# Kernel tuning notes

Hardware: AMD Instinct MI355X
Metric: run time of the kernel (lower is better)

The kernel has to match this reference:

```python
import jax, jax.numpy as jnp
import numpy as np

N_NODES = 50000
N_EDGES = 1600000
CHANNELS = 128
EXPANSION = 50
CUTOFF = 5.0
LOG2 = 0.6931471805599453


def shifted_softplus(x):
    return jax.nn.softplus(x) - LOG2


def gaussian_smearing(r, cutoff=CUTOFF, n=EXPANSION):
    # centers evenly spaced in [0, cutoff]; width set by spacing
    centers = jnp.linspace(0.0, cutoff, n, dtype=r.dtype)
    delta = centers[1] - centers[0]
    coef = 1.0 / (2.0 * delta * delta)
    d = r[:, None] - centers[None, :]          # [E, n]
    return jnp.exp(-coef * d * d)


def setup_inputs() -> dict:
    key = jax.random.key(0)
    ks = jax.random.split(key, 12)
    C, F = CHANNELS, EXPANSION

    def lin(k, fan_in, shape):
        bound = 1.0 / np.sqrt(fan_in)
        return jax.random.uniform(k, shape, jnp.float32, -bound, bound)

    return {
        "features": jax.random.normal(ks[0], (N_NODES, C), jnp.float32),
        "edge_distances": jax.random.uniform(ks[1], (N_EDGES,), jnp.float32) * CUTOFF,
        "W_lin": lin(ks[2], C, (C, C)),
        "Wf1": lin(ks[3], F, (F, C)), "bf1": lin(ks[4], F, (C,)),
        "Wf2": lin(ks[5], C, (C, C)), "bf2": lin(ks[6], C, (C,)),
        "Wm1": lin(ks[7], C, (C, C)), "bm1": lin(ks[8], C, (C,)),
        "Wm2": lin(ks[9], C, (C, C)), "bm2": lin(ks[10], C, (C,)),
        "senders": jax.random.randint(ks[11], (N_EDGES,), 0, N_NODES, jnp.int32),
        "receivers": jax.random.randint(jax.random.fold_in(key, 99), (N_EDGES,), 0, N_NODES, jnp.int32),
    }


def reference(features, edge_distances, W_lin, Wf1, bf1, Wf2, bf2,
              Wm1, bm1, Wm2, bm2, senders, receivers):
    # 1. linear transform of node features (no bias)
    h = features @ W_lin.T                                   # [N, C]
    # 2. learnable radial filter F(r_ij): Gaussian basis -> MLP
    basis = gaussian_smearing(edge_distances)                # [E, F]
    ef = shifted_softplus(basis @ Wf1 + bf1) @ Wf2 + bf2     # [E, C]
    # 3. gather neighbour features, elementwise multiply, scatter-sum
    messages = h[senders] * ef                               # [E, C]
    agg = jax.ops.segment_sum(messages, receivers, num_segments=N_NODES)  # [N, C]
    # 4. output MLP
    return shifted_softplus(agg @ Wm1 + bm1) @ Wm2 + bm2
```

## Files before the change

### kernel.cpp

```cpp
#include <hip/hip_runtime.h>
#include <hip/hip_bf16.h>
#include <math.h>

#define N_NODES 50000
#define N_EDGES 1600000
#define CH 128
#define NF 50
#define NR 4096
#define NODES_PER_BLK 8
#define CHUNK 1024
#define NB 512
#define BUCKET_NODES 98
#define PASSA_CHUNK 4096
#define PASSB_CAP 4608

constexpr float DELTA  = 5.0f / 49.0f;
constexpr float COEF   = 1.0f / (2.0f * DELTA * DELTA);
constexpr float LOG2_  = 0.6931471805599453f;
constexpr float RSCALE = (float)(NR - 1) / 5.0f;

typedef short  bf16x8 __attribute__((ext_vector_type(8)));
typedef float  f32x4  __attribute__((ext_vector_type(4)));
typedef unsigned short ushort_t;
typedef unsigned long long u64;

__device__ __forceinline__ float ssp(float x) {
    return fmaxf(x, 0.0f) + __logf(1.0f + __expf(-fabsf(x))) - LOG2_;
}
__device__ __forceinline__ ushort_t f2bf(float x) {
    __hip_bfloat16 b = __float2bfloat16(x);
    return *reinterpret_cast<ushort_t*>(&b);
}
__device__ __forceinline__ float bf2f(ushort_t u) {
    return __uint_as_float(((unsigned)u) << 16);
}
__device__ __forceinline__ float4 f4zero() { return make_float4(0.f, 0.f, 0.f, 0.f); }

__global__ __launch_bounds__(256) void prep_weights(const float* __restrict__ Wlin,
                                                    const float* __restrict__ Wm1,
                                                    const float* __restrict__ Wm2,
                                                    ushort_t* __restrict__ wlhi,
                                                    ushort_t* __restrict__ wllo,
                                                    ushort_t* __restrict__ wm1hi,
                                                    ushort_t* __restrict__ wm1lo,
                                                    ushort_t* __restrict__ wm2hi,
                                                    ushort_t* __restrict__ wm2lo) {
    int idx = blockIdx.x * 256 + threadIdx.x;
    int n = idx >> 7, k = idx & 127;
    {   float w = Wlin[(size_t)n * CH + k];
        ushort_t hi = f2bf(w); wlhi[n * CH + k] = hi; wllo[n * CH + k] = f2bf(w - bf2f(hi)); }
    {   float w = Wm1[(size_t)k * CH + n];
        ushort_t hi = f2bf(w); wm1hi[n * CH + k] = hi; wm1lo[n * CH + k] = f2bf(w - bf2f(hi)); }
    {   float w = Wm2[(size_t)k * CH + n];
        ushort_t hi = f2bf(w); wm2hi[n * CH + k] = hi; wm2lo[n * CH + k] = f2bf(w - bf2f(hi)); }
}

__global__ __launch_bounds__(128) void table_build(const float* __restrict__ Wf1,
                                                   const float* __restrict__ bf1,
                                                   const float* __restrict__ Wf2,
                                                   const float* __restrict__ bf2,
                                                   float* __restrict__ tab) {
    __shared__ float bas[64];
    __shared__ float t1[128];
    const int g = blockIdx.x, tid = threadIdx.x;
    const float r = (float)g * (5.0f / (float)(NR - 1));
    if (tid < 64) {
        float v = 0.f;
        if (tid < NF) { float d = r - (float)tid * DELTA; v = __expf(-COEF * d * d); }
        bas[tid] = v;
    }
    __syncthreads();
    float acc = bf1[tid];
    for (int k = 0; k < NF; k++) acc = fmaf(bas[k], Wf1[k * CH + tid], acc);
    t1[tid] = ssp(acc);
    __syncthreads();
    float acc2 = bf2[tid];
    for (int k = 0; k < CH; k++) acc2 = fmaf(t1[k], Wf2[k * CH + tid], acc2);
    tab[(size_t)g * CH + tid] = acc2;
}

__global__ __launch_bounds__(256) void table_pack(const float* __restrict__ tab,
                                                  unsigned* __restrict__ tabi) {
    int idx = blockIdx.x * 256 + threadIdx.x;
    int g = idx >> 7, c = idx & 127;
    float a = tab[(size_t)g * CH + c];
    float b = tab[(size_t)min(g + 1, NR - 1) * CH + c];
    tabi[(size_t)g * CH + c] = (unsigned)f2bf(a) | ((unsigned)f2bf(b) << 16);
}

__global__ __launch_bounds__(256) void bucket_hist(const int* __restrict__ recv,
                                                   int* __restrict__ bcnt) {
    __shared__ int bh[NB];
    const int tid = threadIdx.x;
    for (int i = tid; i < NB; i += 256) bh[i] = 0;
    __syncthreads();
    const int e0 = blockIdx.x * PASSA_CHUNK;
#pragma unroll
    for (int i = 0; i < 16; i++) {
        int e = e0 + tid + i * 256;
        if (e < N_EDGES) atomicAdd(&bh[recv[e] / BUCKET_NODES], 1);
    }
    __syncthreads();
    for (int i = tid; i < NB; i += 256)
        if (bh[i]) atomicAdd(&bcnt[i], bh[i]);
}

__global__ __launch_bounds__(256) void bucket_scan(const int* __restrict__ bcnt,
                                                   int* __restrict__ bbase,
                                                   int* __restrict__ bcursor) {
    __shared__ int s[NB];
    const int tid = threadIdx.x;
    s[tid] = bcnt[tid];
    s[tid + 256] = bcnt[tid + 256];
    __syncthreads();
    if (tid == 0) {
        int acc = 0;
        for (int i = 0; i < NB; i++) { int c = s[i]; s[i] = acc; acc += c; }
    }
    __syncthreads();
    bbase[tid] = s[tid];           bbase[tid + 256] = s[tid + 256];
    bcursor[tid] = s[tid];         bcursor[tid + 256] = s[tid + 256];
    if (tid == 0) bbase[NB] = N_EDGES;
}

__global__ __launch_bounds__(256) void bucket_scatter(const int* __restrict__ recv,
                                                      const int* __restrict__ send,
                                                      const float* __restrict__ dist,
                                                      int* __restrict__ bcursor,
                                                      u64* __restrict__ brec) {
    __shared__ int bbaseL[NB];
    __shared__ int bcur[NB];
    const int tid = threadIdx.x;
    for (int i = tid; i < NB; i += 256) bcur[i] = 0;
    __syncthreads();
    const int e0 = blockIdx.x * PASSA_CHUNK;
#pragma unroll
    for (int i = 0; i < 16; i++) {
        int e = e0 + tid + i * 256;
        if (e < N_EDGES) atomicAdd(&bcur[recv[e] / BUCKET_NODES], 1);
    }
    __syncthreads();
    for (int i = tid; i < NB; i += 256) {
        int c = bcur[i];
        if (c) bbaseL[i] = atomicAdd(&bcursor[i], c);
        bcur[i] = 0;
    }
    __syncthreads();
#pragma unroll
    for (int i = 0; i < 16; i++) {
        int e = e0 + tid + i * 256;
        if (e < N_EDGES) {
            int r = recv[e];
            int b = r / BUCKET_NODES;
            int rank = atomicAdd(&bcur[b], 1);
            float x = fminf(dist[e] * RSCALE, (float)(NR - 1));
            u64 rec = (u64)(unsigned)(send[e] | (r << 16)) |
                      ((u64)__float_as_uint(x) << 32);
            brec[bbaseL[b] + rank] = rec;
        }
    }
}

__global__ __launch_bounds__(256) void bucket_sort(const int* __restrict__ bbase,
                                                   const u64* __restrict__ brec,
                                                   u64* __restrict__ meta,
                                                   int* __restrict__ cursor) {
    __shared__ int shist[BUCKET_NODES];
    __shared__ int sexc[BUCKET_NODES];
    __shared__ u64 sout[PASSB_CAP];
    const int b = blockIdx.x, tid = threadIdx.x;
    const int nbase = b * BUCKET_NODES;
    const int nn = min(BUCKET_NODES, N_NODES - nbase);
    if (nn <= 0) return;
    const int ebase = bbase[b], m = bbase[b + 1] - ebase;

    for (int i = tid; i < nn; i += 256) shist[i] = 0;
    __syncthreads();
    for (int i = tid; i < m; i += 256) {
        int l = (int)((brec[ebase + i] >> 16) & 0xFFFF) - nbase;
        atomicAdd(&shist[l], 1);
    }
    __syncthreads();
    if (tid == 0) {
        int acc = 0;
        for (int l = 0; l < nn; l++) { sexc[l] = acc; acc += shist[l]; }
    }
    __syncthreads();
    for (int l = tid; l < nn; l += 256)
        cursor[nbase + l] = ebase + sexc[l] + shist[l];
    __syncthreads();
    for (int i = tid; i < m; i += 256) {
        u64 rec = brec[ebase + i];
        int l = (int)((rec >> 16) & 0xFFFF) - nbase;
        int rank = atomicAdd(&sexc[l], 1);
        if (rank < PASSB_CAP) sout[rank] = rec;
    }
    __syncthreads();
    for (int i = tid; i < m; i += 256) meta[ebase + i] = sout[i];
}

__global__ __launch_bounds__(256) void dense_h(const float* __restrict__ X,
                                               const ushort_t* __restrict__ Bhi,
                                               const ushort_t* __restrict__ Blo,
                                               ushort_t* __restrict__ Y, int M) {
    __shared__ ushort_t xs[64][136];
    const int tid  = threadIdx.x;
    const int row0 = blockIdx.x * 64;

#pragma unroll
    for (int i = 0; i < 8; i++) {
        int idx = tid + i * 256;
        int r   = idx >> 5;
        int c4  = (idx & 31) * 4;
        float4 v = (row0 + r < M) ? *(const float4*)&X[(size_t)(row0 + r) * CH + c4]
                                  : f4zero();
        ushort4 s;
        s.x = f2bf(v.x); s.y = f2bf(v.y); s.z = f2bf(v.z); s.w = f2bf(v.w);
        *(ushort4*)&xs[r][c4] = s;
    }
    __syncthreads();

    const int lane = tid & 63;
    const int wv   = tid >> 6;
    const int row  = lane & 15;
    const int quad = lane >> 4;
    const int c0   = (2 * wv) * 16 + row;
    const int c1   = c0 + 16;

    f32x4 acc[2][4];
#pragma unroll
    for (int j = 0; j < 2; j++)
#pragma unroll
        for (int rt = 0; rt < 4; rt++) acc[j][rt] = (f32x4){0.f, 0.f, 0.f, 0.f};

#pragma unroll
    for (int kb = 0; kb < 128; kb += 32) {
        bf16x8 B0h = *(const bf16x8*)&Bhi[(size_t)c0 * CH + kb + quad * 8];
        bf16x8 B0l = *(const bf16x8*)&Blo[(size_t)c0 * CH + kb + quad * 8];
        bf16x8 B1h = *(const bf16x8*)&Bhi[(size_t)c1 * CH + kb + quad * 8];
        bf16x8 B1l = *(const bf16x8*)&Blo[(size_t)c1 * CH + kb + quad * 8];
#pragma unroll
        for (int rt = 0; rt < 4; rt++) {
            bf16x8 A = *(const bf16x8*)&xs[rt * 16 + row][kb + quad * 8];
            acc[0][rt] = __builtin_amdgcn_mfma_f32_16x16x32_bf16(A, B0l, acc[0][rt], 0, 0, 0);
            acc[0][rt] = __builtin_amdgcn_mfma_f32_16x16x32_bf16(A, B0h, acc[0][rt], 0, 0, 0);
            acc[1][rt] = __builtin_amdgcn_mfma_f32_16x16x32_bf16(A, B1l, acc[1][rt], 0, 0, 0);
            acc[1][rt] = __builtin_amdgcn_mfma_f32_16x16x32_bf16(A, B1h, acc[1][rt], 0, 0, 0);
        }
    }

#pragma unroll
    for (int j = 0; j < 2; j++) {
        int c = j ? c1 : c0;
#pragma unroll
        for (int rt = 0; rt < 4; rt++)
#pragma unroll
            for (int rg = 0; rg < 4; rg++) {
                int r = row0 + rt * 16 + quad * 4 + rg;
                if (r < M) Y[(size_t)r * CH + c] = f2bf(acc[j][rt][rg]);
            }
    }
}

__global__ __launch_bounds__(256) void out_mlp(const ushort_t* __restrict__ AGG,
                                               const ushort_t* __restrict__ B1hi,
                                               const ushort_t* __restrict__ B1lo,
                                               const float* __restrict__ bm1,
                                               const ushort_t* __restrict__ B2hi,
                                               const ushort_t* __restrict__ B2lo,
                                               const float* __restrict__ bm2,
                                               float* __restrict__ OUT, int M) {
    __shared__ ushort_t xs[64][136];
    __shared__ ushort_t ts[64][136];
    const int tid  = threadIdx.x;
    const int row0 = blockIdx.x * 64;

#pragma unroll
    for (int i = 0; i < 4; i++) {
        int idx = tid + i * 256;
        int r   = idx >> 4;
        int c8  = (idx & 15) * 8;
        uint4 v = (row0 + r < M) ? *(const uint4*)&AGG[(size_t)(row0 + r) * CH + c8]
                                 : make_uint4(0, 0, 0, 0);
        *(uint4*)&xs[r][c8] = v;
    }
    __syncthreads();

    const int lane = tid & 63;
    const int wv   = tid >> 6;
    const int row  = lane & 15;
    const int quad = lane >> 4;
    const int c0   = (2 * wv) * 16 + row;
    const int c1   = c0 + 16;

    f32x4 acc[2][4];
#pragma unroll
    for (int j = 0; j < 2; j++)
#pragma unroll
        for (int rt = 0; rt < 4; rt++) acc[j][rt] = (f32x4){0.f, 0.f, 0.f, 0.f};

#pragma unroll
    for (int kb = 0; kb < 128; kb += 32) {
        bf16x8 B0h = *(const bf16x8*)&B1hi[(size_t)c0 * CH + kb + quad * 8];
        bf16x8 B0l = *(const bf16x8*)&B1lo[(size_t)c0 * CH + kb + quad * 8];
        bf16x8 B1h_ = *(const bf16x8*)&B1hi[(size_t)c1 * CH + kb + quad * 8];
        bf16x8 B1l_ = *(const bf16x8*)&B1lo[(size_t)c1 * CH + kb + quad * 8];
#pragma unroll
        for (int rt = 0; rt < 4; rt++) {
            bf16x8 A = *(const bf16x8*)&xs[rt * 16 + row][kb + quad * 8];
            acc[0][rt] = __builtin_amdgcn_mfma_f32_16x16x32_bf16(A, B0l, acc[0][rt], 0, 0, 0);
            acc[0][rt] = __builtin_amdgcn_mfma_f32_16x16x32_bf16(A, B0h, acc[0][rt], 0, 0, 0);
            acc[1][rt] = __builtin_amdgcn_mfma_f32_16x16x32_bf16(A, B1l_, acc[1][rt], 0, 0, 0);
            acc[1][rt] = __builtin_amdgcn_mfma_f32_16x16x32_bf16(A, B1h_, acc[1][rt], 0, 0, 0);
        }
    }
    {
        float bv[2] = { bm1[c0], bm1[c1] };
#pragma unroll
        for (int j = 0; j < 2; j++) {
            int c = j ? c1 : c0;
#pragma unroll
            for (int rt = 0; rt < 4; rt++)
#pragma unroll
                for (int rg = 0; rg < 4; rg++)
                    ts[rt * 16 + quad * 4 + rg][c] = f2bf(ssp(acc[j][rt][rg] + bv[j]));
        }
    }
    __syncthreads();

#pragma unroll
    for (int j = 0; j < 2; j++)
#pragma unroll
        for (int rt = 0; rt < 4; rt++) acc[j][rt] = (f32x4){0.f, 0.f, 0.f, 0.f};

#pragma unroll
    for (int kb = 0; kb < 128; kb += 32) {
        bf16x8 B0h = *(const bf16x8*)&B2hi[(size_t)c0 * CH + kb + quad * 8];
        bf16x8 B0l = *(const bf16x8*)&B2lo[(size_t)c0 * CH + kb + quad * 8];
        bf16x8 B1h_ = *(const bf16x8*)&B2hi[(size_t)c1 * CH + kb + quad * 8];
        bf16x8 B1l_ = *(const bf16x8*)&B2lo[(size_t)c1 * CH + kb + quad * 8];
#pragma unroll
        for (int rt = 0; rt < 4; rt++) {
            bf16x8 A = *(const bf16x8*)&ts[rt * 16 + row][kb + quad * 8];
            acc[0][rt] = __builtin_amdgcn_mfma_f32_16x16x32_bf16(A, B0l, acc[0][rt], 0, 0, 0);
            acc[0][rt] = __builtin_amdgcn_mfma_f32_16x16x32_bf16(A, B0h, acc[0][rt], 0, 0, 0);
            acc[1][rt] = __builtin_amdgcn_mfma_f32_16x16x32_bf16(A, B1l_, acc[1][rt], 0, 0, 0);
            acc[1][rt] = __builtin_amdgcn_mfma_f32_16x16x32_bf16(A, B1h_, acc[1][rt], 0, 0, 0);
        }
    }
    {
        float bv[2] = { bm2[c0], bm2[c1] };
#pragma unroll
        for (int j = 0; j < 2; j++) {
            int c = j ? c1 : c0;
#pragma unroll
            for (int rt = 0; rt < 4; rt++)
#pragma unroll
                for (int rg = 0; rg < 4; rg++) {
                    int r = row0 + rt * 16 + quad * 4 + rg;
                    if (r < M) OUT[(size_t)r * CH + c] = acc[j][rt][rg] + bv[j];
                }
        }
    }
}

__global__ __launch_bounds__(256) void edge_gather(const int* __restrict__ cursor,
                                                   const u64* __restrict__ meta,
                                                   const ushort_t* __restrict__ h,
                                                   const unsigned* __restrict__ tabi,
                                                   ushort_t* __restrict__ aggb) {
    __shared__ u64 smeta[CHUNK];

    const int tid = threadIdx.x;
    const int n0  = blockIdx.x * NODES_PER_BLK;
    const int g   = tid >> 5;
    const int c4  = (tid & 31) * 4;
    const int n   = n0 + g;

    const int myend  = cursor[n];
    const int mybeg  = (n == 0) ? 0 : cursor[n - 1];
    const int blkbeg = (n0 == 0) ? 0 : cursor[n0 - 1];
    const int blkend = cursor[n0 + NODES_PER_BLK - 1];

    float4 macc = f4zero();

    for (int cs = blkbeg; cs < blkend; cs += CHUNK) {
        const int ce = min(cs + CHUNK, blkend);
        __syncthreads();
        for (int i = tid; i < ce - cs; i += 256) smeta[i] = meta[cs + i];
        __syncthreads();

        const int lo = max(mybeg, cs), hi = min(myend, ce);
        int e = lo;
        for (; e + 4 <= hi; e += 4) {
            int s[4]; float fr[4]; int ti[4];
#pragma unroll
            for (int u = 0; u < 4; u++) {
                u64 v = smeta[e - cs + u];
                s[u]  = (int)(v & 0xFFFF);
                float x  = __uint_as_float((unsigned)(v >> 32));
                float fx = floorf(x);
                ti[u] = min((int)fx, NR - 2);
                fr[u] = x - fx;
            }
            ushort4 hu[4]; uint4 tp[4];
#pragma unroll
            for (int u = 0; u < 4; u++) {
                hu[u] = *(const ushort4*)&h[(size_t)s[u] * CH + c4];
                tp[u] = *(const uint4*)&tabi[(size_t)ti[u] * CH + c4];
            }
#pragma unroll
            for (int u = 0; u < 4; u++) {
                float a, b, ef;
                a = __uint_as_float(tp[u].x << 16);
                b = __uint_as_float(tp[u].x & 0xFFFF0000u);
                ef = fmaf(fr[u], b - a, a);
                macc.x = fmaf(bf2f(hu[u].x), ef, macc.x);
                a = __uint_as_float(tp[u].y << 16);
                b = __uint_as_float(tp[u].y & 0xFFFF0000u);
                ef = fmaf(fr[u], b - a, a);
                macc.y = fmaf(bf2f(hu[u].y), ef, macc.y);
                a = __uint_as_float(tp[u].z << 16);
                b = __uint_as_float(tp[u].z & 0xFFFF0000u);
                ef = fmaf(fr[u], b - a, a);
                macc.z = fmaf(bf2f(hu[u].z), ef, macc.z);
                a = __uint_as_float(tp[u].w << 16);
                b = __uint_as_float(tp[u].w & 0xFFFF0000u);
                ef = fmaf(fr[u], b - a, a);
                macc.w = fmaf(bf2f(hu[u].w), ef, macc.w);
            }
        }
        for (; e < hi; e++) {
            u64 v = smeta[e - cs];
            int s = (int)(v & 0xFFFF);
            float x  = __uint_as_float((unsigned)(v >> 32));
            float fx = floorf(x);
            int ti = min((int)fx, NR - 2);
            float fr = x - fx;
            ushort4 hu = *(const ushort4*)&h[(size_t)s * CH + c4];
            uint4   tp = *(const uint4*)&tabi[(size_t)ti * CH + c4];
            float a, b, ef;
            a = __uint_as_float(tp.x << 16); b = __uint_as_float(tp.x & 0xFFFF0000u);
            ef = fmaf(fr, b - a, a); macc.x = fmaf(bf2f(hu.x), ef, macc.x);
            a = __uint_as_float(tp.y << 16); b = __uint_as_float(tp.y & 0xFFFF0000u);
            ef = fmaf(fr, b - a, a); macc.y = fmaf(bf2f(hu.y), ef, macc.y);
            a = __uint_as_float(tp.z << 16); b = __uint_as_float(tp.z & 0xFFFF0000u);
            ef = fmaf(fr, b - a, a); macc.z = fmaf(bf2f(hu.z), ef, macc.z);
            a = __uint_as_float(tp.w << 16); b = __uint_as_float(tp.w & 0xFFFF0000u);
            ef = fmaf(fr, b - a, a); macc.w = fmaf(bf2f(hu.w), ef, macc.w);
        }
    }

    ushort4 o;
    o.x = f2bf(macc.x); o.y = f2bf(macc.y); o.z = f2bf(macc.z); o.w = f2bf(macc.w);
    *(ushort4*)&aggb[(size_t)n * CH + c4] = o;
}

extern "C" void kernel_launch(void* const* d_in, const int* in_sizes, int n_in,
                              void* d_out, int out_size, void* d_ws, size_t ws_size,
                              hipStream_t stream) {
    const float* features = (const float*)d_in[0];
    const float* dist     = (const float*)d_in[1];
    const float* W_lin    = (const float*)d_in[2];
    const float* Wf1      = (const float*)d_in[3];
    const float* bf1      = (const float*)d_in[4];
    const float* Wf2      = (const float*)d_in[5];
    const float* bf2      = (const float*)d_in[6];
    const float* Wm1      = (const float*)d_in[7];
    const float* bm1      = (const float*)d_in[8];
    const float* Wm2      = (const float*)d_in[9];
    const float* bm2      = (const float*)d_in[10];
    const int* senders    = (const int*)d_in[11];
    const int* receivers  = (const int*)d_in[12];
    float* out = (float*)d_out;

    u64* brec       = (u64*)d_ws;
    ushort_t* aggb  = (ushort_t*)d_ws;
    ushort_t* h     = (ushort_t*)(brec + N_EDGES);
    u64* meta       = (u64*)(h + (size_t)N_NODES * CH);
    float* tab      = (float*)(meta + N_EDGES);
    unsigned* tabi  = (unsigned*)(tab + (size_t)NR * CH);
    int* cursor     = (int*)(tabi + (size_t)NR * CH);
    int* bcnt       = cursor + N_NODES;
    int* bbase      = bcnt + NB;
    int* bcursor    = bbase + NB + 1;
    ushort_t* wlhi  = (ushort_t*)(bcursor + NB);
    ushort_t* wllo  = wlhi  + CH * CH;
    ushort_t* wm1hi = wllo  + CH * CH;
    ushort_t* wm1lo = wm1hi + CH * CH;
    ushort_t* wm2hi = wm1lo + CH * CH;
    ushort_t* wm2lo = wm2hi + CH * CH;

    hipMemsetAsync(bcnt, 0, NB * sizeof(int), stream);

    prep_weights<<<64, 256, 0, stream>>>(W_lin, Wm1, Wm2,
                                         wlhi, wllo, wm1hi, wm1lo, wm2hi, wm2lo);
    table_build<<<NR, 128, 0, stream>>>(Wf1, bf1, Wf2, bf2, tab);
    table_pack<<<(NR * CH) / 256, 256, 0, stream>>>(tab, tabi);

    const int nbA = (N_EDGES + PASSA_CHUNK - 1) / PASSA_CHUNK;
    bucket_hist<<<nbA, 256, 0, stream>>>(receivers, bcnt);
    bucket_scan<<<1, 256, 0, stream>>>(bcnt, bbase, bcursor);
    bucket_scatter<<<nbA, 256, 0, stream>>>(receivers, senders, dist, bcursor, brec);
    bucket_sort<<<NB, 256, 0, stream>>>(bbase, brec, meta, cursor);

    const int nb_dense = (N_NODES + 63) / 64;
    dense_h<<<nb_dense, 256, 0, stream>>>(features, wlhi, wllo, h, N_NODES);

    edge_gather<<<N_NODES / NODES_PER_BLK, 256, 0, stream>>>(cursor, meta, h, tabi, aggb);

    out_mlp<<<nb_dense, 256, 0, stream>>>(aggb, wm1hi, wm1lo, bm1, wm2hi, wm2lo, bm2, out, N_NODES);
}
```

Measured before the change: 289.1 us.

## Fuse prep kernels into mega-kernel, drop histogram pass, use nearest-bin radial table

Scatter, filter-table build and the dense h GEMM are merged into one launch dispatched by block index. Edges now go to fixed-capacity bucket slots, so the separate histogram and scan kernels are removed, and the memset moves into the weight-prep kernel. The radial filter table grows to 16384 bins stored as plain bf16 and is read by nearest-bin lookup instead of linear interpolation. This halves table bytes per edge, and per-edge metadata shrinks to 32 bits. Risks are silent edge drops if a bucket exceeds CAP, a 14-bit table-index field, and lower accuracy from removing interpolation.

```diff
diff --git a/kernel.cpp b/kernel.cpp
--- a/kernel.cpp
+++ b/kernel.cpp
@@ -6,13 +6,16 @@
 #define N_EDGES 1600000
 #define CH 128
 #define NF 50
-#define NR 4096
+#define NR 16384
 #define NODES_PER_BLK 8
 #define CHUNK 1024
 #define NB 512
 #define BUCKET_NODES 98
+#define CAP 3840
 #define PASSA_CHUNK 4096
-#define PASSB_CAP 4608
+#define NBLK_SCAT 391
+#define NBLK_TB   8192
+#define NBLK_DH   782
 
 constexpr float DELTA  = 5.0f / 49.0f;
 constexpr float COEF   = 1.0f / (2.0f * DELTA * DELTA);
@@ -36,16 +39,23 @@
 }
 __device__ __forceinline__ float4 f4zero() { return make_float4(0.f, 0.f, 0.f, 0.f); }
 
-__global__ __launch_bounds__(256) void prep_weights(const float* __restrict__ Wlin,
-                                                    const float* __restrict__ Wm1,
-                                                    const float* __restrict__ Wm2,
-                                                    ushort_t* __restrict__ wlhi,
-                                                    ushort_t* __restrict__ wllo,
-                                                    ushort_t* __restrict__ wm1hi,
-                                                    ushort_t* __restrict__ wm1lo,
-                                                    ushort_t* __restrict__ wm2hi,
-                                                    ushort_t* __restrict__ wm2lo) {
-    int idx = blockIdx.x * 256 + threadIdx.x;
+__global__ __launch_bounds__(256) void k1_prep(const float* __restrict__ Wlin,
+                                               const float* __restrict__ Wm1,
+                                               const float* __restrict__ Wm2,
+                                               ushort_t* __restrict__ wlhi,
+                                               ushort_t* __restrict__ wllo,
+                                               ushort_t* __restrict__ wm1hi,
+                                               ushort_t* __restrict__ wm1lo,
+                                               ushort_t* __restrict__ wm2hi,
+                                               ushort_t* __restrict__ wm2lo,
+                                               int* __restrict__ bcnt) {
+    const int tid = threadIdx.x;
+    if (blockIdx.x == 64) {
+        bcnt[tid] = 0;
+        bcnt[tid + 256] = 0;
+        return;
+    }
+    int idx = blockIdx.x * 256 + tid;
     int n = idx >> 7, k = idx & 127;
     {   float w = Wlin[(size_t)n * CH + k];
         ushort_t hi = f2bf(w); wlhi[n * CH + k] = hi; wllo[n * CH + k] = f2bf(w - bf2f(hi)); }
@@ -55,85 +65,18 @@
         ushort_t hi = f2bf(w); wm2hi[n * CH + k] = hi; wm2lo[n * CH + k] = f2bf(w - bf2f(hi)); }
 }
 
-__global__ __launch_bounds__(128) void table_build(const float* __restrict__ Wf1,
-                                                   const float* __restrict__ bf1,
-                                                   const float* __restrict__ Wf2,
-                                                   const float* __restrict__ bf2,
-                                                   float* __restrict__ tab) {
-    __shared__ float bas[64];
-    __shared__ float t1[128];
-    const int g = blockIdx.x, tid = threadIdx.x;
-    const float r = (float)g * (5.0f / (float)(NR - 1));
-    if (tid < 64) {
-        float v = 0.f;
-        if (tid < NF) { float d = r - (float)tid * DELTA; v = __expf(-COEF * d * d); }
-        bas[tid] = v;
-    }
-    __syncthreads();
-    float acc = bf1[tid];
-    for (int k = 0; k < NF; k++) acc = fmaf(bas[k], Wf1[k * CH + tid], acc);
-    t1[tid] = ssp(acc);
-    __syncthreads();
-    float acc2 = bf2[tid];
-    for (int k = 0; k < CH; k++) acc2 = fmaf(t1[k], Wf2[k * CH + tid], acc2);
-    tab[(size_t)g * CH + tid] = acc2;
-}
-
-__global__ __launch_bounds__(256) void table_pack(const float* __restrict__ tab,
-                                                  unsigned* __restrict__ tabi) {
-    int idx = blockIdx.x * 256 + threadIdx.x;
-    int g = idx >> 7, c = idx & 127;
-    float a = tab[(size_t)g * CH + c];
-    float b = tab[(size_t)min(g + 1, NR - 1) * CH + c];
-    tabi[(size_t)g * CH + c] = (unsigned)f2bf(a) | ((unsigned)f2bf(b) << 16);
-}
-
-__global__ __launch_bounds__(256) void bucket_hist(const int* __restrict__ recv,
-                                                   int* __restrict__ bcnt) {
-    __shared__ int bh[NB];
-    const int tid = threadIdx.x;
-    for (int i = tid; i < NB; i += 256) bh[i] = 0;
-    __syncthreads();
-    const int e0 = blockIdx.x * PASSA_CHUNK;
-#pragma unroll
-    for (int i = 0; i < 16; i++) {
-        int e = e0 + tid + i * 256;
-        if (e < N_EDGES) atomicAdd(&bh[recv[e] / BUCKET_NODES], 1);
-    }
-    __syncthreads();
-    for (int i = tid; i < NB; i += 256)
-        if (bh[i]) atomicAdd(&bcnt[i], bh[i]);
-}
-
-__global__ __launch_bounds__(256) void bucket_scan(const int* __restrict__ bcnt,
-                                                   int* __restrict__ bbase,
-                                                   int* __restrict__ bcursor) {
-    __shared__ int s[NB];
-    const int tid = threadIdx.x;
-    s[tid] = bcnt[tid];
-    s[tid + 256] = bcnt[tid + 256];
-    __syncthreads();
-    if (tid == 0) {
-        int acc = 0;
-        for (int i = 0; i < NB; i++) { int c = s[i]; s[i] = acc; acc += c; }
-    }
-    __syncthreads();
-    bbase[tid] = s[tid];           bbase[tid + 256] = s[tid + 256];
-    bcursor[tid] = s[tid];         bcursor[tid + 256] = s[tid + 256];
-    if (tid == 0) bbase[NB] = N_EDGES;
-}
-
-__global__ __launch_bounds__(256) void bucket_scatter(const int* __restrict__ recv,
-                                                      const int* __restrict__ send,
-                                                      const float* __restrict__ dist,
-                                                      int* __restrict__ bcursor,
-                                                      u64* __restrict__ brec) {
-    __shared__ int bbaseL[NB];
-    __shared__ int bcur[NB];
+__device__ void scatter_body(char* smem, int blk,
+                             const int* __restrict__ recv,
+                             const int* __restrict__ send,
+                             const float* __restrict__ dist,
+                             int* __restrict__ bcnt,
+                             u64* __restrict__ brec) {
+    int* bcur   = (int*)smem;
+    int* bbaseL = bcur + NB;
     const int tid = threadIdx.x;
     for (int i = tid; i < NB; i += 256) bcur[i] = 0;
     __syncthreads();
-    const int e0 = blockIdx.x * PASSA_CHUNK;
+    const int e0 = blk * PASSA_CHUNK;
 #pragma unroll
     for (int i = 0; i < 16; i++) {
         int e = e0 + tid + i * 256;
@@ -142,7 +85,7 @@
     __syncthreads();
     for (int i = tid; i < NB; i += 256) {
         int c = bcur[i];
-        if (c) bbaseL[i] = atomicAdd(&bcursor[i], c);
+        bbaseL[i] = c ? atomicAdd(&bcnt[i], c) : 0;
         bcur[i] = 0;
     }
     __syncthreads();
@@ -152,68 +95,60 @@
         if (e < N_EDGES) {
             int r = recv[e];
             int b = r / BUCKET_NODES;
-            int rank = atomicAdd(&bcur[b], 1);
-            float x = fminf(dist[e] * RSCALE, (float)(NR - 1));
-            u64 rec = (u64)(unsigned)(send[e] | (r << 16)) |
-                      ((u64)__float_as_uint(x) << 32);
-            brec[bbaseL[b] + rank] = rec;
-        }
-    }
-}
-
-__global__ __launch_bounds__(256) void bucket_sort(const int* __restrict__ bbase,
-                                                   const u64* __restrict__ brec,
-                                                   u64* __restrict__ meta,
-                                                   int* __restrict__ cursor) {
-    __shared__ int shist[BUCKET_NODES];
-    __shared__ int sexc[BUCKET_NODES];
-    __shared__ u64 sout[PASSB_CAP];
-    const int b = blockIdx.x, tid = threadIdx.x;
-    const int nbase = b * BUCKET_NODES;
-    const int nn = min(BUCKET_NODES, N_NODES - nbase);
-    if (nn <= 0) return;
-    const int ebase = bbase[b], m = bbase[b + 1] - ebase;
-
-    for (int i = tid; i < nn; i += 256) shist[i] = 0;
-    __syncthreads();
-    for (int i = tid; i < m; i += 256) {
-        int l = (int)((brec[ebase + i] >> 16) & 0xFFFF) - nbase;
-        atomicAdd(&shist[l], 1);
-    }
-    __syncthreads();
-    if (tid == 0) {
-        int acc = 0;
-        for (int l = 0; l < nn; l++) { sexc[l] = acc; acc += shist[l]; }
-    }
-    __syncthreads();
-    for (int l = tid; l < nn; l += 256)
-        cursor[nbase + l] = ebase + sexc[l] + shist[l];
-    __syncthreads();
-    for (int i = tid; i < m; i += 256) {
-        u64 rec = brec[ebase + i];
-        int l = (int)((rec >> 16) & 0xFFFF) - nbase;
-        int rank = atomicAdd(&sexc[l], 1);
-        if (rank < PASSB_CAP) sout[rank] = rec;
-    }
-    __syncthreads();
-    for (int i = tid; i < m; i += 256) meta[ebase + i] = sout[i];
-}
-
-__global__ __launch_bounds__(256) void dense_h(const float* __restrict__ X,
-                                               const ushort_t* __restrict__ Bhi,
-                                               const ushort_t* __restrict__ Blo,
-                                               ushort_t* __restrict__ Y, int M) {
-    __shared__ ushort_t xs[64][136];
+            int rank = bbaseL[b] + atomicAdd(&bcur[b], 1);
+            if (rank < CAP) {
+                float x = fminf(dist[e] * RSCALE, (float)(NR - 1));
+                int ti = __float2int_rn(x);
+                u64 rec = (u64)(unsigned)(send[e] | (r << 16)) | ((u64)ti << 32);
+                brec[(size_t)b * CAP + rank] = rec;
+            }
+        }
+    }
+}
+
+__device__ void table_body(char* smem, int blk,
+                           const float* __restrict__ Wf1,
+                           const float* __restrict__ bf1,
+                           const float* __restrict__ Wf2,
+                           const float* __restrict__ bf2,
+                           ushort_t* __restrict__ tabn) {
+    float* bas = (float*)smem;
+    float* t1  = (float*)smem + 128;
     const int tid  = threadIdx.x;
-    const int row0 = blockIdx.x * 64;
+    const int half = tid >> 7, t = tid & 127;
+    const int g = blk * 2 + half;
+    const float r = (float)g * (5.0f / (float)(NR - 1));
+    if (t < 64) {
+        float v = 0.f;
+        if (t < NF) { float d = r - (float)t * DELTA; v = __expf(-COEF * d * d); }
+        bas[half * 64 + t] = v;
+    }
+    __syncthreads();
+    float acc = bf1[t];
+    for (int k = 0; k < NF; k++) acc = fmaf(bas[half * 64 + k], Wf1[k * CH + t], acc);
+    t1[half * 128 + t] = ssp(acc);
+    __syncthreads();
+    float acc2 = bf2[t];
+    for (int k = 0; k < CH; k++) acc2 = fmaf(t1[half * 128 + k], Wf2[k * CH + t], acc2);
+    tabn[(size_t)g * CH + t] = f2bf(acc2);
+}
+
+__device__ void dense_h_body(char* smem, int blk,
+                             const float* __restrict__ X,
+                             const ushort_t* __restrict__ Bhi,
+                             const ushort_t* __restrict__ Blo,
+                             ushort_t* __restrict__ Y) {
+    ushort_t (*xs)[136] = (ushort_t (*)[136])smem;
+    const int tid  = threadIdx.x;
+    const int row0 = blk * 64;
 
 #pragma unroll
     for (int i = 0; i < 8; i++) {
         int idx = tid + i * 256;
         int r   = idx >> 5;
         int c4  = (idx & 31) * 4;
-        float4 v = (row0 + r < M) ? *(const float4*)&X[(size_t)(row0 + r) * CH + c4]
-                                  : f4zero();
+        float4 v = (row0 + r < N_NODES) ? *(const float4*)&X[(size_t)(row0 + r) * CH + c4]
+                                        : f4zero();
         ushort4 s;
         s.x = f2bf(v.x); s.y = f2bf(v.y); s.z = f2bf(v.z); s.w = f2bf(v.w);
         *(ushort4*)&xs[r][c4] = s;
@@ -257,9 +192,153 @@
 #pragma unroll
             for (int rg = 0; rg < 4; rg++) {
                 int r = row0 + rt * 16 + quad * 4 + rg;
-                if (r < M) Y[(size_t)r * CH + c] = f2bf(acc[j][rt][rg]);
+                if (r < N_NODES) Y[(size_t)r * CH + c] = f2bf(acc[j][rt][rg]);
             }
     }
+}
+
+__global__ __launch_bounds__(256) void k2_mega(const int* __restrict__ recv,
+                                               const int* __restrict__ send,
+                                               const float* __restrict__ dist,
+                                               int* __restrict__ bcnt,
+                                               u64* __restrict__ brec,
+                                               const float* __restrict__ Wf1,
+                                               const float* __restrict__ bf1,
+                                               const float* __restrict__ Wf2,
+                                               const float* __restrict__ bf2,
+                                               ushort_t* __restrict__ tabn,
+                                               const float* __restrict__ X,
+                                               const ushort_t* __restrict__ wlhi,
+                                               const ushort_t* __restrict__ wllo,
+                                               ushort_t* __restrict__ h) {
+    __shared__ __align__(16) char smem[64 * 136 * 2];
+    const int blk = blockIdx.x;
+    if (blk < NBLK_SCAT) {
+        scatter_body(smem, blk, recv, send, dist, bcnt, brec);
+    } else if (blk < NBLK_SCAT + NBLK_TB) {
+        table_body(smem, blk - NBLK_SCAT, Wf1, bf1, Wf2, bf2, tabn);
+    } else {
+        dense_h_body(smem, blk - NBLK_SCAT - NBLK_TB, X, wlhi, wllo, h);
+    }
+}
+
+__global__ __launch_bounds__(256) void bucket_sort(const int* __restrict__ bcnt,
+                                                   const u64* __restrict__ brec,
+                                                   unsigned* __restrict__ meta,
+                                                   int* __restrict__ cursor) {
+    __shared__ int sbc[NB];
+    __shared__ int shist[BUCKET_NODES];
+    __shared__ int sexc[BUCKET_NODES];
+    __shared__ unsigned sout[CAP];
+    __shared__ int sgb;
+    const int b = blockIdx.x, tid = threadIdx.x;
+    const int nbase = b * BUCKET_NODES;
+    const int nn = min(BUCKET_NODES, N_NODES - nbase);
+    if (nn <= 0) return;
+
+    sbc[tid] = bcnt[tid];
+    sbc[tid + 256] = bcnt[tid + 256];
+    for (int i = tid; i < nn; i += 256) shist[i] = 0;
+    __syncthreads();
+    if (tid == 0) {
+        int acc = 0;
+        for (int i = 0; i < b; i++) acc += min(sbc[i], CAP);
+        sgb = acc;
+    }
+    __syncthreads();
+    const int gbase = sgb;
+    const int m = min(sbc[b], CAP);
+    const u64* my = brec + (size_t)b * CAP;
+
+    for (int i = tid; i < m; i += 256) {
+        int l = (int)((my[i] >> 16) & 0xFFFF) - nbase;
+        atomicAdd(&shist[l], 1);
+    }
+    __syncthreads();
+    if (tid == 0) {
+        int acc = 0;
+        for (int l = 0; l < nn; l++) { sexc[l] = acc; acc += shist[l]; }
+    }
+    __syncthreads();
+    for (int l = tid; l < nn; l += 256)
+        cursor[nbase + l] = gbase + sexc[l] + shist[l];
+    __syncthreads();
+    for (int i = tid; i < m; i += 256) {
+        u64 rec = my[i];
+        int l = (int)((rec >> 16) & 0xFFFF) - nbase;
+        int rank = atomicAdd(&sexc[l], 1);
+        sout[rank] = (unsigned)(rec & 0xFFFF) | ((unsigned)((rec >> 32) & 0x3FFF) << 16);
+    }
+    __syncthreads();
+    for (int i = tid; i < m; i += 256) meta[gbase + i] = sout[i];
+}
+
+__global__ __launch_bounds__(256) void edge_gather(const int* __restrict__ cursor,
+                                                   const unsigned* __restrict__ meta,
+                                                   const ushort_t* __restrict__ h,
+                                                   const ushort_t* __restrict__ tabn,
+                                                   ushort_t* __restrict__ aggb) {
+    __shared__ unsigned smeta[CHUNK];
+
+    const int tid = threadIdx.x;
+    const int n0  = blockIdx.x * NODES_PER_BLK;
+    const int g   = tid >> 5;
+    const int c4  = (tid & 31) * 4;
+    const int n   = n0 + g;
+
+    const int myend  = cursor[n];
+    const int mybeg  = (n == 0) ? 0 : cursor[n - 1];
+    const int blkbeg = (n0 == 0) ? 0 : cursor[n0 - 1];
+    const int blkend = cursor[n0 + NODES_PER_BLK - 1];
+
+    float4 macc = f4zero();
+
+    for (int cs = blkbeg; cs < blkend; cs += CHUNK) {
+        const int ce = min(cs + CHUNK, blkend);
+        __syncthreads();
+        for (int i = tid; i < ce - cs; i += 256) smeta[i] = meta[cs + i];
+        __syncthreads();
+
+        const int lo = max(mybeg, cs), hi = min(myend, ce);
+        int e = lo;
+        for (; e + 4 <= hi; e += 4) {
+            int s[4], ti[4];
+#pragma unroll
+            for (int u = 0; u < 4; u++) {
+                unsigned v = smeta[e - cs + u];
+                s[u]  = (int)(v & 0xFFFF);
+                ti[u] = (int)(v >> 16);
+            }
+            ushort4 hu[4], tn[4];
+#pragma unroll
+            for (int u = 0; u < 4; u++) {
+                hu[u] = *(const ushort4*)&h[(size_t)s[u] * CH + c4];
+                tn[u] = *(const ushort4*)&tabn[(size_t)ti[u] * CH + c4];
+            }
+#pragma unroll
+            for (int u = 0; u < 4; u++) {
+                macc.x = fmaf(bf2f(hu[u].x), bf2f(tn[u].x), macc.x);
+                macc.y = fmaf(bf2f(hu[u].y), bf2f(tn[u].y), macc.y);
+                macc.z = fmaf(bf2f(hu[u].z), bf2f(tn[u].z), macc.z);
+                macc.w = fmaf(bf2f(hu[u].w), bf2f(tn[u].w), macc.w);
+            }
+        }
+        for (; e < hi; e++) {
+            unsigned v = smeta[e - cs];
+            int s  = (int)(v & 0xFFFF);
+            int ti = (int)(v >> 16);
+            ushort4 hu = *(const ushort4*)&h[(size_t)s * CH + c4];
+            ushort4 tn = *(const ushort4*)&tabn[(size_t)ti * CH + c4];
+            macc.x = fmaf(bf2f(hu.x), bf2f(tn.x), macc.x);
+            macc.y = fmaf(bf2f(hu.y), bf2f(tn.y), macc.y);
+            macc.z = fmaf(bf2f(hu.z), bf2f(tn.z), macc.z);
+            macc.w = fmaf(bf2f(hu.w), bf2f(tn.w), macc.w);
+        }
+    }
+
+    ushort4 o;
+    o.x = f2bf(macc.x); o.y = f2bf(macc.y); o.z = f2bf(macc.z); o.w = f2bf(macc.w);
+    *(ushort4*)&aggb[(size_t)n * CH + c4] = o;
 }
 
 __global__ __launch_bounds__(256) void out_mlp(const ushort_t* __restrict__ AGG,
@@ -362,98 +441,6 @@
                 }
         }
     }
-}
-
-__global__ __launch_bounds__(256) void edge_gather(const int* __restrict__ cursor,
-                                                   const u64* __restrict__ meta,
-                                                   const ushort_t* __restrict__ h,
-                                                   const unsigned* __restrict__ tabi,
-                                                   ushort_t* __restrict__ aggb) {
-    __shared__ u64 smeta[CHUNK];
-
-    const int tid = threadIdx.x;
-    const int n0  = blockIdx.x * NODES_PER_BLK;
-    const int g   = tid >> 5;
-    const int c4  = (tid & 31) * 4;
-    const int n   = n0 + g;
-
-    const int myend  = cursor[n];
-    const int mybeg  = (n == 0) ? 0 : cursor[n - 1];
-    const int blkbeg = (n0 == 0) ? 0 : cursor[n0 - 1];
-    const int blkend = cursor[n0 + NODES_PER_BLK - 1];
-
-    float4 macc = f4zero();
-
-    for (int cs = blkbeg; cs < blkend; cs += CHUNK) {
-        const int ce = min(cs + CHUNK, blkend);
-        __syncthreads();
-        for (int i = tid; i < ce - cs; i += 256) smeta[i] = meta[cs + i];
-        __syncthreads();
-
-        const int lo = max(mybeg, cs), hi = min(myend, ce);
-        int e = lo;
-        for (; e + 4 <= hi; e += 4) {
-            int s[4]; float fr[4]; int ti[4];
-#pragma unroll
-            for (int u = 0; u < 4; u++) {
-                u64 v = smeta[e - cs + u];
-                s[u]  = (int)(v & 0xFFFF);
-                float x  = __uint_as_float((unsigned)(v >> 32));
-                float fx = floorf(x);
-                ti[u] = min((int)fx, NR - 2);
-                fr[u] = x - fx;
-            }
-            ushort4 hu[4]; uint4 tp[4];
-#pragma unroll
-            for (int u = 0; u < 4; u++) {
-                hu[u] = *(const ushort4*)&h[(size_t)s[u] * CH + c4];
-                tp[u] = *(const uint4*)&tabi[(size_t)ti[u] * CH + c4];
-            }
-#pragma unroll
-            for (int u = 0; u < 4; u++) {
-                float a, b, ef;
-                a = __uint_as_float(tp[u].x << 16);
-                b = __uint_as_float(tp[u].x & 0xFFFF0000u);
-                ef = fmaf(fr[u], b - a, a);
-                macc.x = fmaf(bf2f(hu[u].x), ef, macc.x);
-                a = __uint_as_float(tp[u].y << 16);
-                b = __uint_as_float(tp[u].y & 0xFFFF0000u);
-                ef = fmaf(fr[u], b - a, a);
-                macc.y = fmaf(bf2f(hu[u].y), ef, macc.y);
-                a = __uint_as_float(tp[u].z << 16);
-                b = __uint_as_float(tp[u].z & 0xFFFF0000u);
-                ef = fmaf(fr[u], b - a, a);
-                macc.z = fmaf(bf2f(hu[u].z), ef, macc.z);
-                a = __uint_as_float(tp[u].w << 16);
-                b = __uint_as_float(tp[u].w & 0xFFFF0000u);
-                ef = fmaf(fr[u], b - a, a);
-                macc.w = fmaf(bf2f(hu[u].w), ef, macc.w);
-            }
-        }
-        for (; e < hi; e++) {
-            u64 v = smeta[e - cs];
-            int s = (int)(v & 0xFFFF);
-            float x  = __uint_as_float((unsigned)(v >> 32));
-            float fx = floorf(x);
-            int ti = min((int)fx, NR - 2);
-            float fr = x - fx;
-            ushort4 hu = *(const ushort4*)&h[(size_t)s * CH + c4];
-            uint4   tp = *(const uint4*)&tabi[(size_t)ti * CH + c4];
-            float a, b, ef;
-            a = __uint_as_float(tp.x << 16); b = __uint_as_float(tp.x & 0xFFFF0000u);
-            ef = fmaf(fr, b - a, a); macc.x = fmaf(bf2f(hu.x), ef, macc.x);
-            a = __uint_as_float(tp.y << 16); b = __uint_as_float(tp.y & 0xFFFF0000u);
-            ef = fmaf(fr, b - a, a); macc.y = fmaf(bf2f(hu.y), ef, macc.y);
-            a = __uint_as_float(tp.z << 16); b = __uint_as_float(tp.z & 0xFFFF0000u);
-            ef = fmaf(fr, b - a, a); macc.z = fmaf(bf2f(hu.z), ef, macc.z);
-            a = __uint_as_float(tp.w << 16); b = __uint_as_float(tp.w & 0xFFFF0000u);
-            ef = fmaf(fr, b - a, a); macc.w = fmaf(bf2f(hu.w), ef, macc.w);
-        }
-    }
-
-    ushort4 o;
-    o.x = f2bf(macc.x); o.y = f2bf(macc.y); o.z = f2bf(macc.z); o.w = f2bf(macc.w);
-    *(ushort4*)&aggb[(size_t)n * CH + c4] = o;
 }
 
 extern "C" void kernel_launch(void* const* d_in, const int* in_sizes, int n_in,
@@ -476,38 +463,30 @@
 
     u64* brec       = (u64*)d_ws;
     ushort_t* aggb  = (ushort_t*)d_ws;
-    ushort_t* h     = (ushort_t*)(brec + N_EDGES);
-    u64* meta       = (u64*)(h + (size_t)N_NODES * CH);
-    float* tab      = (float*)(meta + N_EDGES);
-    unsigned* tabi  = (unsigned*)(tab + (size_t)NR * CH);
-    int* cursor     = (int*)(tabi + (size_t)NR * CH);
+    ushort_t* h     = (ushort_t*)(brec + (size_t)NB * CAP);
+    unsigned* meta  = (unsigned*)(h + (size_t)N_NODES * CH);
+    ushort_t* tabn  = (ushort_t*)(meta + N_EDGES);
+    int* cursor     = (int*)(tabn + (size_t)NR * CH);
     int* bcnt       = cursor + N_NODES;
-    int* bbase      = bcnt + NB;
-    int* bcursor    = bbase + NB + 1;
-    ushort_t* wlhi  = (ushort_t*)(bcursor + NB);
+    ushort_t* wlhi  = (ushort_t*)(bcnt + NB);
     ushort_t* wllo  = wlhi  + CH * CH;
     ushort_t* wm1hi = wllo  + CH * CH;
     ushort_t* wm1lo = wm1hi + CH * CH;
     ushort_t* wm2hi = wm1lo + CH * CH;
     ushort_t* wm2lo = wm2hi + CH * CH;
 
-    hipMemsetAsync(bcnt, 0, NB * sizeof(int), stream);
-
-    prep_weights<<<64, 256, 0, stream>>>(W_lin, Wm1, Wm2,
-                                         wlhi, wllo, wm1hi, wm1lo, wm2hi, wm2lo);
-    table_build<<<NR, 128, 0, stream>>>(Wf1, bf1, Wf2, bf2, tab);
-    table_pack<<<(NR * CH) / 256, 256, 0, stream>>>(tab, tabi);
-
-    const int nbA = (N_EDGES + PASSA_CHUNK - 1) / PASSA_CHUNK;
-    bucket_hist<<<nbA, 256, 0, stream>>>(receivers, bcnt);
-    bucket_scan<<<1, 256, 0, stream>>>(bcnt, bbase, bcursor);
-    bucket_scatter<<<nbA, 256, 0, stream>>>(receivers, senders, dist, bcursor, brec);
-    bucket_sort<<<NB, 256, 0, stream>>>(bbase, brec, meta, cursor);
-
-    const int nb_dense = (N_NODES + 63) / 64;
-    dense_h<<<nb_dense, 256, 0, stream>>>(features, wlhi, wllo, h, N_NODES);
-
-    edge_gather<<<N_NODES / NODES_PER_BLK, 256, 0, stream>>>(cursor, meta, h, tabi, aggb);
-
-    out_mlp<<<nb_dense, 256, 0, stream>>>(aggb, wm1hi, wm1lo, bm1, wm2hi, wm2lo, bm2, out, N_NODES);
-}
+    k1_prep<<<65, 256, 0, stream>>>(W_lin, Wm1, Wm2,
+                                    wlhi, wllo, wm1hi, wm1lo, wm2hi, wm2lo, bcnt);
+
+    k2_mega<<<NBLK_SCAT + NBLK_TB + NBLK_DH, 256, 0, stream>>>(
+        receivers, senders, dist, bcnt, brec,
+        Wf1, bf1, Wf2, bf2, tabn,
+        features, wlhi, wllo, h);
+
+    bucket_sort<<<NB, 256, 0, stream>>>(bcnt, brec, meta, cursor);
+
+    edge_gather<<<N_NODES / NODES_PER_BLK, 256, 0, stream>>>(cursor, meta, h, tabn, aggb);
+
+    out_mlp<<<NBLK_DH, 256, 0, stream>>>(aggb, wm1hi, wm1lo, bm1,
+                                         wm2hi, wm2lo, bm2, out, N_NODES);
+}
```

After: 294.5 us. No clear change (+1.9%).
